# Optimization experiments

Hardware: AMD Instinct MI355X
Metric: run time of the kernel (lower is better)

The kernel has to match this reference:

```python
import jax, jax.numpy as jnp
import numpy as np

B, D, T, STRIDE = 16, 512, 2048, 4
SIGMA_SQUARE = 5.0
L = -(-T // STRIDE)  # ceil(T/stride) = 512


def setup_inputs() -> dict:
    key = jax.random.key(0)
    k1, k2, k3 = jax.random.split(key, 3)
    x = jax.random.normal(k1, (B, D, T), dtype=jnp.float32)
    # score conv: Conv1d(hdim, 1, 1, bias=False) == a single weight vector over D
    # (zero-initialized in the module; use small random values for a meaningful test)
    w = jax.random.normal(k2, (D,), dtype=jnp.float32) * 0.01
    x_lengths = jax.random.randint(k3, (B,), T // 2, T + 1)
    x_mask = jnp.arange(T)[None, :] < x_lengths[:, None]  # [B, T] bool
    return {"x": x, "w": w, "x_mask": x_mask, "x_lengths": x_lengths}


def reference(x, w, x_mask, x_lengths):
    maskf = x_mask.astype(x.dtype)  # [B, T]
    z_lengths = jnp.ceil(x_lengths.astype(x.dtype) / STRIDE).astype(jnp.int32)  # [B]
    z_mask = x_mask[:, ::STRIDE]  # [B, L]

    # score = exp(conv1x1(x)) * mask ; cum-sum position score
    score = jnp.exp(jnp.einsum('bdt,d->bt', x, w)) * maskf  # [B, T]
    cum = jnp.cumsum(score, axis=-1)  # [B, T]
    norm = (cum - cum[:, :1]) / (cum[:, -1:] - cum[:, :1]) \
           * (z_lengths[:, None].astype(x.dtype) - 1.0)  # [B, T]

    # monotonic-rate regularizer (get_score_loss)
    diff = norm[:, 1:] - norm[:, :-1]  # [B, T-1]
    score_loss = ((jax.nn.relu(diff - 1.0) * maskf[:, 1:]).sum(axis=-1)
                  / (x_lengths.astype(x.dtype) - 1.0)).mean()

    # masked Gaussian distance -> softmax over T -> alignment-weighted sum
    idx = jnp.arange(L, dtype=x.dtype)  # [L]
    dist = -SIGMA_SQUARE * (idx[None, None, :] - norm[:, :, None]) ** 2  # [B, T, L]
    dist = jnp.swapaxes(dist, 1, 2)  # [B, L, T]
    dist = jnp.where(x_mask[:, None, :], dist, -jnp.inf)
    alignment = jax.nn.softmax(dist, axis=-1) * z_mask[:, :, None].astype(x.dtype)  # [B, L, T]

    z = jnp.einsum('blt,bdt->bdl', alignment, x)  # [B, D, L]
    return z, z_mask, z_lengths, alignment, score_loss
```

## Files before the change

### kernel.cpp

```cpp
#include <hip/hip_runtime.h>
#include <cstddef>

#define Bn 16
#define Dn 512
#define Tn 2048
#define Ln 512
#define NLT 64

__global__ __launch_bounds__(256) void score_kernel(const float* __restrict__ x,
                                                    const float* __restrict__ w,
                                                    const int* __restrict__ xlen,
                                                    float* __restrict__ score) {
    int blk = blockIdx.x;
    int b   = blk >> 5;
    int tc  = blk & 31;
    int tid = threadIdx.x;
    int xl  = xlen[b];
    int t0c = tc * 64;
    if (t0c >= xl) {
        if (tid < 16)
            *(float4*)&score[b * Tn + t0c + tid * 4] = make_float4(0.f, 0.f, 0.f, 0.f);
        return;
    }
    int tq  = tid & 15;
    int dg  = tid >> 4;
    int t0  = t0c + tq * 4;
    const float* xb = x + (size_t)b * Dn * Tn + t0;
    float4 acc = make_float4(0.f, 0.f, 0.f, 0.f);
    int dbase = dg * 32;
#pragma unroll 8
    for (int i = 0; i < 32; ++i) {
        int d = dbase + i;
        float4 v = *(const float4*)&xb[(size_t)d * Tn];
        float wd = w[d];
        acc.x = fmaf(v.x, wd, acc.x);
        acc.y = fmaf(v.y, wd, acc.y);
        acc.z = fmaf(v.z, wd, acc.z);
        acc.w = fmaf(v.w, wd, acc.w);
    }
    __shared__ float4 red[16][16];
    red[dg][tq] = acc;
    __syncthreads();
    if (tid < 16) {
        float4 s = red[0][tid];
#pragma unroll
        for (int g = 1; g < 16; ++g) {
            float4 r = red[g][tid];
            s.x += r.x; s.y += r.y; s.z += r.z; s.w += r.w;
        }
        int t = t0c + tid * 4;
        float4 o;
        o.x = (t + 0 < xl) ? __expf(s.x) : 0.f;
        o.y = (t + 1 < xl) ? __expf(s.y) : 0.f;
        o.z = (t + 2 < xl) ? __expf(s.z) : 0.f;
        o.w = (t + 3 < xl) ? __expf(s.w) : 0.f;
        *(float4*)&score[b * Tn + t] = o;
    }
}

__global__ __launch_bounds__(256) void scan_kernel(const float* __restrict__ score,
                                                   const int* __restrict__ xlen,
                                                   float* __restrict__ norm,
                                                   float* __restrict__ loss_part,
                                                   float* __restrict__ zmask_out,
                                                   float* __restrict__ zlen_out,
                                                   int* __restrict__ wlo,
                                                   int* __restrict__ whi,
                                                   float* __restrict__ sMout,
                                                   float* __restrict__ sIout) {
    int b = blockIdx.x, tid = threadIdx.x;
    int xl = xlen[b];
    int zl = (xl + 3) >> 2;
    const float* sc = score + b * Tn;

    __shared__ float sNorm[Tn];
    __shared__ int   sTC[Ln];

    float v[8]; float s = 0.f;
#pragma unroll
    for (int k = 0; k < 8; ++k) { v[k] = sc[tid * 8 + k]; s += v[k]; }

    float ps = s;
#pragma unroll
    for (int off = 1; off < 64; off <<= 1) {
        float n = __shfl_up(ps, off, 64);
        if ((tid & 63) >= off) ps += n;
    }
    __shared__ float wsum[4];
    if ((tid & 63) == 63) wsum[tid >> 6] = ps;
    __syncthreads();
    float base = 0.f;
#pragma unroll
    for (int wv = 0; wv < 4; ++wv) if (wv < (tid >> 6)) base += wsum[wv];
    float total = wsum[0] + wsum[1] + wsum[2] + wsum[3];
    float cum0  = sc[0];
    float scale = (float)(zl - 1) / (total - cum0);

    float run = base + ps - s;
    float nv[8];
#pragma unroll
    for (int k = 0; k < 8; ++k) {
        run += v[k];
        float xx = (run - cum0) * scale;
        nv[k] = xx;
        norm[b * Tn + tid * 8 + k] = xx;
        sNorm[tid * 8 + k] = xx;
    }

    float ls = 0.f;
#pragma unroll
    for (int k = 0; k < 8; ++k) {
        int t = tid * 8 + k;
        if (t >= 1 && t < xl) {
            float diff = v[k] * scale;
            ls += fmaxf(diff - 1.0f, 0.f);
        }
    }
#pragma unroll
    for (int off = 32; off; off >>= 1) ls += __shfl_down(ls, off, 64);
    __shared__ float lw[4];
    if ((tid & 63) == 0) lw[tid >> 6] = ls;

    for (int l = tid; l < Ln; l += 256)
        zmask_out[b * Ln + l] = (l * 4 < xl) ? 1.f : 0.f;
    if (tid == 0) zlen_out[b] = (float)zl;

    for (int i = tid; i < NLT; i += 256) {
        wlo[b * NLT + i] = xl;
        whi[b * NLT + i] = xl;
    }
    for (int l = tid; l < Ln; l += 256) sTC[l] = xl - 1;
    __syncthreads();
    if (tid == 0) loss_part[b] = (lw[0] + lw[1] + lw[2] + lw[3]) / (float)(xl - 1);

#pragma unroll
    for (int k = 0; k < 8; ++k) {
        int t = tid * 8 + k;
        float vv = nv[k];
        float p  = (t == 0) ? -1e9f : sNorm[t - 1];
        int lsr = (int)floorf((p + 1.5f) * 0.125f) + 1; if (lsr < 0) lsr = 0;
        int ler = (int)floorf((vv + 1.5f) * 0.125f);    if (ler > NLT - 1) ler = NLT - 1;
        for (int lt = lsr; lt <= ler; ++lt) wlo[b * NLT + lt] = t;
        int hs = (int)ceilf((p - 8.5f) * 0.125f);       if (hs < 0) hs = 0;
        int he = (int)ceilf((vv - 8.5f) * 0.125f) - 1;  if (he > NLT - 1) he = NLT - 1;
        for (int lt = hs; lt <= he; ++lt) whi[b * NLT + lt] = t;
        int cs = (int)floorf(p) + 1;  if (cs < 0) cs = 0;
        int ce = (int)floorf(vv);     if (ce > Ln - 1) ce = Ln - 1;
        for (int l = cs; l <= ce; ++l) sTC[l] = t;
    }
    __syncthreads();

    for (int l = tid; l < Ln; l += 256) {
        float mv = 0.f, iv = 0.f;
        if (l < zl) {
            int tc2 = sTC[l];
            float d1 = (float)l - sNorm[tc2];
            float m  = -5.f * d1 * d1;
            if (tc2 > 0) { float d0v = (float)l - sNorm[tc2 - 1]; float c = -5.f * d0v * d0v; m = fmaxf(m, c); }
            int lo = (l >= 2) ? sTC[l - 2] : 0;
            int hi = (l + 2 <= zl - 1) ? sTC[l + 2] : xl;
            int tcm1 = (tc2 > 0) ? tc2 - 1 : 0;
            if (lo > tcm1) lo = tcm1;
            int tcp1 = (tc2 + 1 < xl) ? tc2 + 1 : xl;
            if (hi < tcp1) hi = tcp1;
            float ssum = 0.f;
            for (int t = lo; t < hi; ++t) {
                float df = (float)l - sNorm[t];
                ssum += __expf(-5.f * df * df - m);
            }
            mv = m; iv = 1.f / ssum;
        }
        sMout[b * Ln + l] = mv;
        sIout[b * Ln + l] = iv;
    }
}

__global__ __launch_bounds__(256) void z_kernel(const float* __restrict__ x,
                                                const float* __restrict__ norm,
                                                const int* __restrict__ xlen,
                                                const int* __restrict__ wlo,
                                                const int* __restrict__ whi,
                                                const float* __restrict__ sM,
                                                const float* __restrict__ sI,
                                                float* __restrict__ z) {
    int tid = threadIdx.x;
    int bid = blockIdx.x;
    int swz = (bid & 7) * 256 + (bid >> 3);
    int b   = swz >> 7;
    int rem = swz & 127;
    int lt  = rem >> 1;
    int dh  = rem & 1;
    int l0  = lt * 8;
    int xl  = xlen[b];
    int zl  = (xl + 3) >> 2;
    int d   = dh * 256 + tid;
    size_t zr = (size_t)(b * Dn + d) * Ln + l0;

    if (l0 >= zl) {
        float4 z4 = make_float4(0.f, 0.f, 0.f, 0.f);
        *(float4*)&z[zr] = z4; *(float4*)&z[zr + 4] = z4;
        return;
    }

    int tlo = wlo[b * NLT + lt];
    int thi = whi[b * NLT + lt];
    if (thi > xl) thi = xl;
    int tA = tlo & ~15;

    __shared__ float sA[64][8];
    const float* nb = norm + b * Tn;
    const float* xr = x + (size_t)(b * Dn + d) * Tn;

    int al = tid >> 5;
    int as = tid & 31;
    float ml = sM[b * Ln + l0 + al];
    float il = sI[b * Ln + l0 + al];
    float lr = (float)(l0 + al);

    float acc[8] = {};
    float4 rx[16];

    for (int t0 = tA; t0 < thi; t0 += 64) {
#pragma unroll
        for (int j = 0; j < 16; ++j) {
            int tj = t0 + 4 * j;
            if (tj > Tn - 4) tj = Tn - 4;
            rx[j] = *(const float4*)&xr[tj];
        }
        {
            int t1 = t0 + as, t2 = t1 + 32;
            float a1 = 0.f, a2 = 0.f;
            if (t1 < thi) { float df = lr - nb[t1]; a1 = __expf(fmaf(-5.f * df, df, -ml)) * il; }
            if (t2 < thi) { float df = lr - nb[t2]; a2 = __expf(fmaf(-5.f * df, df, -ml)) * il; }
            sA[as][al] = a1;
            sA[as + 32][al] = a2;
        }
        __syncthreads();
#pragma unroll
        for (int c = 0; c < 16; ++c) {
            float4 xv = rx[c];
#pragma unroll
            for (int e = 0; e < 4; ++e) {
                int s = 4 * c + e;
                float xs = ((const float*)&xv)[e];
                float4 a0 = *(const float4*)&sA[s][0];
                float4 a1 = *(const float4*)&sA[s][4];
                acc[0] = fmaf(xs, a0.x, acc[0]);
                acc[1] = fmaf(xs, a0.y, acc[1]);
                acc[2] = fmaf(xs, a0.z, acc[2]);
                acc[3] = fmaf(xs, a0.w, acc[3]);
                acc[4] = fmaf(xs, a1.x, acc[4]);
                acc[5] = fmaf(xs, a1.y, acc[5]);
                acc[6] = fmaf(xs, a1.z, acc[6]);
                acc[7] = fmaf(xs, a1.w, acc[7]);
            }
        }
        __syncthreads();
    }

    *(float4*)&z[zr]     = make_float4(acc[0], acc[1], acc[2], acc[3]);
    *(float4*)&z[zr + 4] = make_float4(acc[4], acc[5], acc[6], acc[7]);
}

__global__ __launch_bounds__(256) void align_kernel(const float* __restrict__ norm,
                                                    const int* __restrict__ xlen,
                                                    const float* __restrict__ sM,
                                                    const float* __restrict__ sI,
                                                    const float* __restrict__ loss_part,
                                                    float* __restrict__ align,
                                                    float* __restrict__ out_loss) {
    int tid = threadIdx.x;
    int bid = blockIdx.x;
    if (bid == 0 && tid == 0) {
        float s = 0.f;
        for (int i = 0; i < Bn; ++i) s += loss_part[i];
        out_loss[0] = s / (float)Bn;
    }
    int swz = (bid & 7) * 512 + (bid >> 3);
    int b   = swz >> 8;
    int rp  = swz & 255;
    int l0a = rp * 2;
    int xl  = xlen[b];
    const float* nb = norm + b * Tn;
    float ml0 = sM[b * Ln + l0a],     il0 = sI[b * Ln + l0a];
    float ml1 = sM[b * Ln + l0a + 1], il1 = sI[b * Ln + l0a + 1];
    float lr0 = (float)l0a, lr1 = (float)(l0a + 1);
    float* a0p = align + (size_t)(b * Ln + l0a) * Tn;
    float* a1p = a0p + Tn;
#pragma unroll
    for (int h = 0; h < 2; ++h) {
        int t = 4 * tid + h * 1024;
        float4 nv = *(const float4*)&nb[t];
        float4 o0, o1;
        float d0, d1;
#define AVAL(J, E, NJ)                                                         \
        d0 = lr0 - (NJ); d1 = lr1 - (NJ);                                      \
        o0.J = (t + (E) < xl) ? __expf(fmaf(-5.f * d0, d0, -ml0)) * il0 : 0.f; \
        o1.J = (t + (E) < xl) ? __expf(fmaf(-5.f * d1, d1, -ml1)) * il1 : 0.f;
        AVAL(x, 0, nv.x) AVAL(y, 1, nv.y) AVAL(z, 2, nv.z) AVAL(w, 3, nv.w)
#undef AVAL
        *(float4*)&a0p[t] = o0;
        *(float4*)&a1p[t] = o1;
    }
}

extern "C" void kernel_launch(void* const* d_in, const int* in_sizes, int n_in,
                              void* d_out, int out_size, void* d_ws, size_t ws_size,
                              hipStream_t stream) {
    const float* x    = (const float*)d_in[0];
    const float* w    = (const float*)d_in[1];
    const int*   xlen = (const int*)d_in[3];
    float* out = (float*)d_out;

    const size_t OFF_Z     = 0;
    const size_t OFF_ZMASK = (size_t)Bn * Dn * Ln;
    const size_t OFF_ZLEN  = OFF_ZMASK + (size_t)Bn * Ln;
    const size_t OFF_ALIGN = OFF_ZLEN + Bn;
    const size_t OFF_LOSS  = OFF_ALIGN + (size_t)Bn * Ln * Tn;

    float* score     = (float*)d_ws;
    float* norm      = score + (size_t)Bn * Tn;
    float* loss_part = norm + (size_t)Bn * Tn;
    int*   wlo       = (int*)(loss_part + Bn);
    int*   whi       = wlo + Bn * NLT;
    float* sMw       = (float*)(whi + Bn * NLT);
    float* sIw       = sMw + (size_t)Bn * Ln;

    score_kernel<<<Bn * 32, 256, 0, stream>>>(x, w, xlen, score);
    scan_kernel<<<Bn, 256, 0, stream>>>(score, xlen, norm, loss_part,
                                        out + OFF_ZMASK, out + OFF_ZLEN,
                                        wlo, whi, sMw, sIw);
    z_kernel<<<Bn * NLT * 2, 256, 0, stream>>>(x, norm, xlen, wlo, whi,
                                               sMw, sIw, out + OFF_Z);
    align_kernel<<<Bn * Ln / 2, 256, 0, stream>>>(norm, xlen, sMw, sIw, loss_part,
                                                  out + OFF_ALIGN, out + OFF_LOSS);
}
```

Measured before the change: 57.98 us.

## Fuse alignment writes into z kernel and zero-fill alignment with bulk kernel

Removes the standalone align kernel, which evaluated the Gaussian softmax over every (l, t) pair. A simple float4 zero-fill kernel now clears the whole alignment tensor first. The z kernel then writes the nonzero window values it already computes for its shared-memory tile. This avoids recomputing exps and reading norm for full rows. In exchange it adds scattered scalar stores inside z_kernel and still writes the full alignment buffer once via the fill. The loss reduction moves into z_kernel.

```diff
diff --git a/kernel.cpp b/kernel.cpp
--- a/kernel.cpp
+++ b/kernel.cpp
@@ -6,6 +6,16 @@
 #define Tn 2048
 #define Ln 512
 #define NLT 64
+
+__global__ __launch_bounds__(256) void fill_kernel(float4* __restrict__ align4) {
+    const size_t NT = (size_t)Bn * Ln * Tn / 16;
+    size_t i = (size_t)blockIdx.x * 256 + threadIdx.x;
+    float4 z4 = make_float4(0.f, 0.f, 0.f, 0.f);
+    align4[i]          = z4;
+    align4[i + NT]     = z4;
+    align4[i + 2 * NT] = z4;
+    align4[i + 3 * NT] = z4;
+}
 
 __global__ __launch_bounds__(256) void score_kernel(const float* __restrict__ x,
                                                     const float* __restrict__ w,
@@ -182,9 +192,17 @@
                                                 const int* __restrict__ whi,
                                                 const float* __restrict__ sM,
                                                 const float* __restrict__ sI,
-                                                float* __restrict__ z) {
+                                                const float* __restrict__ loss_part,
+                                                float* __restrict__ align,
+                                                float* __restrict__ z,
+                                                float* __restrict__ out_loss) {
     int tid = threadIdx.x;
     int bid = blockIdx.x;
+    if (bid == 0 && tid == 0) {
+        float s = 0.f;
+        for (int i = 0; i < Bn; ++i) s += loss_part[i];
+        out_loss[0] = s / (float)Bn;
+    }
     int swz = (bid & 7) * 256 + (bid >> 3);
     int b   = swz >> 7;
     int rem = swz & 127;
@@ -216,6 +234,7 @@
     float ml = sM[b * Ln + l0 + al];
     float il = sI[b * Ln + l0 + al];
     float lr = (float)(l0 + al);
+    float* ar = align + (size_t)(b * Ln + l0 + al) * Tn;
 
     float acc[8] = {};
     float4 rx[16];
@@ -234,6 +253,10 @@
             if (t2 < thi) { float df = lr - nb[t2]; a2 = __expf(fmaf(-5.f * df, df, -ml)) * il; }
             sA[as][al] = a1;
             sA[as + 32][al] = a2;
+            if (dh == 0) {
+                if (t1 < thi) ar[t1] = a1;
+                if (t2 < thi) ar[t2] = a2;
+            }
         }
         __syncthreads();
 #pragma unroll
@@ -262,48 +285,6 @@
     *(float4*)&z[zr + 4] = make_float4(acc[4], acc[5], acc[6], acc[7]);
 }
 
-__global__ __launch_bounds__(256) void align_kernel(const float* __restrict__ norm,
-                                                    const int* __restrict__ xlen,
-                                                    const float* __restrict__ sM,
-                                                    const float* __restrict__ sI,
-                                                    const float* __restrict__ loss_part,
-                                                    float* __restrict__ align,
-                                                    float* __restrict__ out_loss) {
-    int tid = threadIdx.x;
-    int bid = blockIdx.x;
-    if (bid == 0 && tid == 0) {
-        float s = 0.f;
-        for (int i = 0; i < Bn; ++i) s += loss_part[i];
-        out_loss[0] = s / (float)Bn;
-    }
-    int swz = (bid & 7) * 512 + (bid >> 3);
-    int b   = swz >> 8;
-    int rp  = swz & 255;
-    int l0a = rp * 2;
-    int xl  = xlen[b];
-    const float* nb = norm + b * Tn;
-    float ml0 = sM[b * Ln + l0a],     il0 = sI[b * Ln + l0a];
-    float ml1 = sM[b * Ln + l0a + 1], il1 = sI[b * Ln + l0a + 1];
-    float lr0 = (float)l0a, lr1 = (float)(l0a + 1);
-    float* a0p = align + (size_t)(b * Ln + l0a) * Tn;
-    float* a1p = a0p + Tn;
-#pragma unroll
-    for (int h = 0; h < 2; ++h) {
-        int t = 4 * tid + h * 1024;
-        float4 nv = *(const float4*)&nb[t];
-        float4 o0, o1;
-        float d0, d1;
-#define AVAL(J, E, NJ)                                                         \
-        d0 = lr0 - (NJ); d1 = lr1 - (NJ);                                      \
-        o0.J = (t + (E) < xl) ? __expf(fmaf(-5.f * d0, d0, -ml0)) * il0 : 0.f; \
-        o1.J = (t + (E) < xl) ? __expf(fmaf(-5.f * d1, d1, -ml1)) * il1 : 0.f;
-        AVAL(x, 0, nv.x) AVAL(y, 1, nv.y) AVAL(z, 2, nv.z) AVAL(w, 3, nv.w)
-#undef AVAL
-        *(float4*)&a0p[t] = o0;
-        *(float4*)&a1p[t] = o1;
-    }
-}
-
 extern "C" void kernel_launch(void* const* d_in, const int* in_sizes, int n_in,
                               void* d_out, int out_size, void* d_ws, size_t ws_size,
                               hipStream_t stream) {
@@ -326,12 +307,13 @@
     float* sMw       = (float*)(whi + Bn * NLT);
     float* sIw       = sMw + (size_t)Bn * Ln;
 
+    fill_kernel<<<4096, 256, 0, stream>>>((float4*)(out + OFF_ALIGN));
     score_kernel<<<Bn * 32, 256, 0, stream>>>(x, w, xlen, score);
     scan_kernel<<<Bn, 256, 0, stream>>>(score, xlen, norm, loss_part,
                                         out + OFF_ZMASK, out + OFF_ZLEN,
                                         wlo, whi, sMw, sIw);
     z_kernel<<<Bn * NLT * 2, 256, 0, stream>>>(x, norm, xlen, wlo, whi,
-                                               sMw, sIw, out + OFF_Z);
-    align_kernel<<<Bn * Ln / 2, 256, 0, stream>>>(norm, xlen, sMw, sIw, loss_part,
-                                                  out + OFF_ALIGN, out + OFF_LOSS);
-}
+                                               sMw, sIw, loss_part,
+                                               out + OFF_ALIGN, out + OFF_Z,
+                                               out + OFF_LOSS);
+}
```

Measured after the change: 58.41 us. No clear change (+0.7%).
